# Performance work log

Hardware: AMD Instinct MI355X
Metric: run time of the kernel (lower is better)

Reference implementation:

```python
import jax, jax.numpy as jnp
import numpy as np

N_ITER = 2


def _ssn_iter(pixel_features, sh, sw, n_iter=N_ITER):
    """Faithful JAX port of ssn_iter: returns dense abs_affinity (B, ns, N).

    dist[b,k,p] = ||pix[b,:,p] - spix[b,:,cand_k(p)]||^2 over the 3x3 superpixel
    neighborhood of each pixel's initial label; invalid candidates get +inf
    (softmax -> 0), matching the CUDA PairwiseDistFunction + mask semantics.
    """
    B, C, H, W = pixel_features.shape
    nsh, nsw = H // sh, W // sw
    ns = nsh * nsw
    N = H * W

    # calc_init_centroid: adaptive_avg_pool2d == block mean when divisible
    spix = pixel_features.reshape(B, C, nsh, sh, nsw, sw).mean(axis=(3, 5)).reshape(B, C, ns)

    # init_label_map via nearest interpolation == (row//sh)*nsw + col//sw
    r0 = jnp.repeat(jnp.arange(H) // sh, W)            # (N,) superpixel row of each pixel
    c0 = jnp.tile(jnp.arange(W) // sw, H)              # (N,) superpixel col

    # 9 candidate offsets, ordered as [r-nsw, r, r+nsw] with r in [-1,0,1]
    dr = jnp.repeat(jnp.arange(-1, 2), 3)              # (9,)
    dc = jnp.tile(jnp.arange(-1, 2), 3)                # (9,)
    rr = r0[None, :] + dr[:, None]                     # (9, N)
    cc = c0[None, :] + dc[:, None]                     # (9, N)
    valid = (rr >= 0) & (rr < nsh) & (cc >= 0) & (cc < nsw)   # (9, N)
    sidx = jnp.clip(rr * nsw + cc, 0, ns - 1)          # (9, N) candidate superpixel ids
    pidx = jnp.broadcast_to(jnp.arange(N), (9, N))     # (9, N) pixel ids

    pf = pixel_features.reshape(B, C, N)

    def scatter_dense(a):  # a: (9, N) affinity -> dense (ns, N)
        return jnp.zeros((ns, N), a.dtype).at[sidx, pidx].add(a)

    abs_aff = None
    for k in range(n_iter):
        g = spix[:, :, sidx.reshape(-1)].reshape(B, C, 9, N)          # gather candidates
        d = ((pf[:, :, None, :] - g) ** 2).sum(axis=1)                # (B, 9, N)
        d = jnp.where(valid[None], d, jnp.inf)
        aff = jax.nn.softmax(-d, axis=1)                              # invalid -> 0
        aff = jnp.where(valid[None], aff, 0.0)
        abs_aff = jax.vmap(scatter_dense)(aff)                        # (B, ns, N)
        if k < n_iter - 1:
            num = jnp.einsum('bsn,bcn->bsc', abs_aff, pf)             # dense bmm
            den = abs_aff.sum(axis=2)[..., None] + 1e-16
            spix = (num / den).transpose(0, 2, 1)                     # (B, C, ns)
    return abs_aff


def setup_inputs() -> dict:
    key = jax.random.key(0)
    x = jax.random.normal(key, (2, 64, 320, 320), dtype=jnp.float32)
    return {"pixel_features": x, "stoken_h": 16, "stoken_w": 16}


def reference(pixel_features, stoken_h, stoken_w):
    return _ssn_iter(pixel_features, stoken_h, stoken_w, N_ITER)
```

## Files before the change

kernel.cpp:

```cpp
#include <hip/hip_runtime.h>

#define KB   2
#define KC   64
#define KH   320
#define KW   320
#define KSH  16
#define KSW  16
#define KNSH 20
#define KNSW 20
#define KNS  400
#define KN   102400

#define TOTF4  20480000u
#define Z1     6800000u
#define Z2     13640000u
#define NZA    1024
#define NZB    1248
#define NZC    1248
#define NCOMPA 2560
#define NCOMP  800

typedef float float4v __attribute__((ext_vector_type(4)));

__global__ __launch_bounds__(320) void block_mean_kernel(
    const float* __restrict__ pf, float* __restrict__ spix,
    float* __restrict__ outz) {
  if (blockIdx.x < NZA) {
    unsigned tid = blockIdx.x * 320u + threadIdx.x;
    const unsigned stride = NZA * 320u;
    float4v z = (float4v)(0.f);
    float4v* o = (float4v*)outz;
    for (unsigned i = tid; i < Z1; i += stride)
      __builtin_nontemporal_store(z, &o[i]);
    return;
  }
  int wg = blockIdx.x - NZA;
  int rb = wg % KNSH;
  int c  = (wg / KNSH) % KC;
  int b  = wg / (KNSH * KC);
  int t  = threadIdx.x;

  const float* row0 = pf + ((size_t)(b * KC + c) * KH + rb * KSH) * KW;
  float acc = 0.f;
#pragma unroll
  for (int i = 0; i < KSH; ++i) acc += row0[i * KW + t];

#pragma unroll
  for (int off = 8; off > 0; off >>= 1) acc += __shfl_down(acc, off, 16);

  if ((t & 15) == 0)
    spix[(b * KC + c) * KNS + rb * KNSW + (t >> 4)] = acc * (1.0f / (KSH * KSW));
}

__global__ __launch_bounds__(256) void dist_partial_kernel(
    const float* __restrict__ pf, const float* __restrict__ spix,
    float* __restrict__ part, float* __restrict__ den,
    float* __restrict__ outz) {
  if (blockIdx.x < NZB) {
    unsigned tid = blockIdx.x * 256u + threadIdx.x;
    const unsigned stride = NZB * 256u;
    float4v z = (float4v)(0.f);
    float4v* o = (float4v*)outz;
    for (unsigned i = Z1 + tid; i < Z2; i += stride)
      __builtin_nontemporal_store(z, &o[i]);
    return;
  }

  __shared__ float scand[9][KC];
  __shared__ __align__(16) float aff_s[9][256];
  __shared__ float part_s[9][64];
  __shared__ float den_s[9];

  int wg = blockIdx.x - NZB;
  int s  = wg % KNS;
  int b  = wg / KNS;
  int sr = s / KNSW, sc = s % KNSW;
  int t  = threadIdx.x;

  for (int idx = t; idx < 9 * KC; idx += 256) {
    int k = idx >> 6, c = idx & 63;
    int rr = sr + k / 3 - 1, cc = sc + k % 3 - 1;
    float v = 0.f;
    if (rr >= 0 && rr < KNSH && cc >= 0 && cc < KNSW)
      v = spix[(b * KC + c) * KNS + rr * KNSW + cc];
    scand[k][c] = v;
  }
  __syncthreads();

  int ti = t >> 4, tj = t & 15;
  int p = (sr * KSH + ti) * KW + sc * KSW + tj;
  const float* pfp = pf + (size_t)b * KC * KN + p;

  float d[9];
#pragma unroll
  for (int k = 0; k < 9; ++k) d[k] = 0.f;
  for (int c = 0; c < KC; ++c) {
    float x = pfp[(size_t)c * KN];
#pragma unroll
    for (int k = 0; k < 9; ++k) {
      float df = x - scand[k][c];
      d[k] = fmaf(df, df, d[k]);
    }
  }
  float m = 3.4e38f;
#pragma unroll
  for (int k = 0; k < 9; ++k) {
    int rr = sr + k / 3 - 1, cc = sc + k % 3 - 1;
    if (rr >= 0 && rr < KNSH && cc >= 0 && cc < KNSW) m = fminf(m, d[k]);
  }
  float e[9];
  float sum = 0.f;
#pragma unroll
  for (int k = 0; k < 9; ++k) {
    int rr = sr + k / 3 - 1, cc = sc + k % 3 - 1;
    bool valid = (rr >= 0 && rr < KNSH && cc >= 0 && cc < KNSW);
    e[k] = valid ? __expf(m - d[k]) : 0.f;
    sum += e[k];
  }
  float inv = 1.0f / sum;
#pragma unroll
  for (int k = 0; k < 9; ++k) aff_s[k][t] = e[k] * inv;
  __syncthreads();

  int w = t >> 6, l = t & 63;
  int li = l >> 2, lj4 = (l & 3) * 4;
  const float* pfb = pf + ((size_t)b * KC + w * 16) * KN
                   + (sr * KSH + li) * KW + sc * KSW + lj4;

  const float4v a0 = *(const float4v*)(&aff_s[0][l * 4]);
  const float4v a1 = *(const float4v*)(&aff_s[1][l * 4]);
  const float4v a2 = *(const float4v*)(&aff_s[2][l * 4]);
  const float4v a3 = *(const float4v*)(&aff_s[3][l * 4]);
  const float4v a4 = *(const float4v*)(&aff_s[4][l * 4]);
  const float4v a5 = *(const float4v*)(&aff_s[5][l * 4]);
  const float4v a6 = *(const float4v*)(&aff_s[6][l * 4]);
  const float4v a7 = *(const float4v*)(&aff_s[7][l * 4]);
  const float4v a8 = *(const float4v*)(&aff_s[8][l * 4]);

  if (w == 0) {
#define DENK(k, av)                                                       \
    {                                                                     \
      float dv = (av.x + av.y) + (av.z + av.w);                           \
      _Pragma("unroll")                                                   \
      for (int off = 32; off > 0; off >>= 1) dv += __shfl_xor(dv, off, 64); \
      if (l == 0) den_s[k] = dv;                                          \
    }
    DENK(0, a0) DENK(1, a1) DENK(2, a2) DENK(3, a3) DENK(4, a4)
    DENK(5, a5) DENK(6, a6) DENK(7, a7) DENK(8, a8)
#undef DENK
  }

#pragma unroll
  for (int cb = 0; cb < 4; ++cb) {
    float4v x0 = *(const float4v*)(pfb + (size_t)(cb * 4 + 0) * KN);
    float4v x1 = *(const float4v*)(pfb + (size_t)(cb * 4 + 1) * KN);
    float4v x2 = *(const float4v*)(pfb + (size_t)(cb * 4 + 2) * KN);
    float4v x3 = *(const float4v*)(pfb + (size_t)(cb * 4 + 3) * KN);

    float acc[4][9];
#define DOTS(c, xv)                                                        \
    acc[c][0] = fmaf(xv.x, a0.x, fmaf(xv.y, a0.y, fmaf(xv.z, a0.z, xv.w * a0.w))); \
    acc[c][1] = fmaf(xv.x, a1.x, fmaf(xv.y, a1.y, fmaf(xv.z, a1.z, xv.w * a1.w))); \
    acc[c][2] = fmaf(xv.x, a2.x, fmaf(xv.y, a2.y, fmaf(xv.z, a2.z, xv.w * a2.w))); \
    acc[c][3] = fmaf(xv.x, a3.x, fmaf(xv.y, a3.y, fmaf(xv.z, a3.z, xv.w * a3.w))); \
    acc[c][4] = fmaf(xv.x, a4.x, fmaf(xv.y, a4.y, fmaf(xv.z, a4.z, xv.w * a4.w))); \
    acc[c][5] = fmaf(xv.x, a5.x, fmaf(xv.y, a5.y, fmaf(xv.z, a5.z, xv.w * a5.w))); \
    acc[c][6] = fmaf(xv.x, a6.x, fmaf(xv.y, a6.y, fmaf(xv.z, a6.z, xv.w * a6.w))); \
    acc[c][7] = fmaf(xv.x, a7.x, fmaf(xv.y, a7.y, fmaf(xv.z, a7.z, xv.w * a7.w))); \
    acc[c][8] = fmaf(xv.x, a8.x, fmaf(xv.y, a8.y, fmaf(xv.z, a8.z, xv.w * a8.w)));
    DOTS(0, x0) DOTS(1, x1) DOTS(2, x2) DOTS(3, x3)
#undef DOTS

#pragma unroll
    for (int off = 32; off > 0; off >>= 1)
#pragma unroll
      for (int c = 0; c < 4; ++c)
#pragma unroll
        for (int k = 0; k < 9; ++k)
          acc[c][k] += __shfl_xor(acc[c][k], off, 64);

    if (l == 0) {
#pragma unroll
      for (int c = 0; c < 4; ++c)
#pragma unroll
        for (int k = 0; k < 9; ++k)
          part_s[k][w * 16 + cb * 4 + c] = acc[c][k];
    }
  }
  __syncthreads();

  size_t base = ((size_t)b * KNS + s) * 9;
  for (int idx = t; idx < 9 * 64; idx += 256)
    part[base * 64 + idx] = part_s[idx >> 6][idx & 63];
  if (t < 9) den[base + t] = den_s[t];
}

__global__ __launch_bounds__(256) void dist_band_kernel(
    const float* __restrict__ pf, const float* __restrict__ part,
    const float* __restrict__ den, float* __restrict__ out) {
  if (blockIdx.x < NZC) {
    unsigned tid = blockIdx.x * 256u + threadIdx.x;
    const unsigned stride = NZC * 256u;
    float4v z = (float4v)(0.f);
    float4v* o = (float4v*)out;
    for (unsigned i = Z2 + tid; i < TOTF4; i += stride) {
      unsigned orow = i / 25600u;
      unsigned f4   = i - orow * 25600u;
      unsigned s    = orow % KNS;
      unsigned p    = f4 * 4u;
      int sr = (int)(s / KNSW), sc = (int)(s % KNSW);
      int r0 = (int)(p / 5120u);
      int c0 = (int)((p % KW) >> 4);
      int dr = sr - r0, dc = sc - c0;
      if (dr < -1 || dr > 1 || dc < -1 || dc > 1)
        __builtin_nontemporal_store(z, &o[i]);
    }
    return;
  }

  __shared__ float scand[9][KC];

  int wg = blockIdx.x - NZC;
  int s  = wg % KNS;
  int b  = wg / KNS;
  int sr = s / KNSW, sc = s % KNSW;
  int t  = threadIdx.x;

  for (int idx = t; idx < 9 * KC; idx += 256) {
    int k = idx >> 6, c = idx & 63;
    int nr = sr + k / 3 - 1, nc = sc + k % 3 - 1;
    float v = 0.f;
    if (nr >= 0 && nr < KNSH && nc >= 0 && nc < KNSW) {
      float num = 0.f, dsum = 0.f;
#pragma unroll
      for (int j = 0; j < 9; ++j) {
        int rr = nr + j / 3 - 1, cc = nc + j % 3 - 1;
        if (rr >= 0 && rr < KNSH && cc >= 0 && cc < KNSW) {
          size_t base = ((size_t)b * KNS + rr * KNSW + cc) * 9 + (8 - j);
          num  += part[base * 64 + c];
          dsum += den[base];
        }
      }
      v = num / (dsum + 1e-16f);
    }
    scand[k][c] = v;
  }
  __syncthreads();

  int i = t >> 4, j = t & 15;
  int p = (sr * KSH + i) * KW + sc * KSW + j;
  const float* pfb = pf + (size_t)b * KC * KN + p;

  float d[9];
#pragma unroll
  for (int k = 0; k < 9; ++k) d[k] = 0.f;

  for (int c = 0; c < KC; ++c) {
    float x = pfb[(size_t)c * KN];
#pragma unroll
    for (int k = 0; k < 9; ++k) {
      float df = x - scand[k][c];
      d[k] = fmaf(df, df, d[k]);
    }
  }

  float m = 3.4e38f;
#pragma unroll
  for (int k = 0; k < 9; ++k) {
    int rr = sr + k / 3 - 1, cc = sc + k % 3 - 1;
    bool valid = (rr >= 0 && rr < KNSH && cc >= 0 && cc < KNSW);
    if (valid) m = fminf(m, d[k]);
  }
  float e[9];
  float sum = 0.f;
#pragma unroll
  for (int k = 0; k < 9; ++k) {
    int rr = sr + k / 3 - 1, cc = sc + k % 3 - 1;
    bool valid = (rr >= 0 && rr < KNSH && cc >= 0 && cc < KNSW);
    e[k] = valid ? __expf(m - d[k]) : 0.f;
    sum += e[k];
  }
  float inv = 1.0f / sum;

#pragma unroll
  for (int k = 0; k < 9; ++k) {
    int rr = sr + k / 3 - 1, cc = sc + k % 3 - 1;
    if (rr >= 0 && rr < KNSH && cc >= 0 && cc < KNSW)
      __builtin_nontemporal_store(e[k] * inv,
          out + ((size_t)b * KNS + rr * KNSW + cc) * KN + p);
  }
}

extern "C" void kernel_launch(void* const* d_in, const int* in_sizes, int n_in,
                              void* d_out, int out_size, void* d_ws, size_t ws_size,
                              hipStream_t stream) {
  const float* pf = (const float*)d_in[0];
  float* out = (float*)d_out;

  float* spix0 = (float*)d_ws;
  float* partw = spix0 + (size_t)KB * KC * KNS;
  float* denw  = partw + (size_t)KB * KNS * 9 * 64;

  block_mean_kernel<<<NZA + NCOMPA, 320, 0, stream>>>(pf, spix0, out);
  dist_partial_kernel<<<NZB + NCOMP, 256, 0, stream>>>(pf, spix0, partw, denw, out);
  dist_band_kernel<<<NZC + NCOMP, 256, 0, stream>>>(pf, partw, denw, out);
}
```

Measured before the change: 144.9 us.

## Move output zeroing out of band kernel and dispatch compute blocks first

The pass that zero-fills the huge dense output is now split evenly between the first two kernels, each covering half the buffer unconditionally. The third kernel no longer zeroes anything and only writes the banded affinities. Compute workgroups now sit at the low block indices so they are dispatched ahead of the zero-fill blocks. This drops the per-element band test and its integer divisions from the zero loop, but the band region is now written twice and the last kernel's compute no longer overlaps with any zeroing.

```diff
diff --git a/kernel.cpp b/kernel.cpp
--- a/kernel.cpp
+++ b/kernel.cpp
@@ -12,29 +12,27 @@
 #define KN   102400
 
 #define TOTF4  20480000u
-#define Z1     6800000u
-#define Z2     13640000u
+#define HALF4  10240000u
+#define NCOMPA 2560
 #define NZA    1024
+#define NCOMP  800
 #define NZB    1248
-#define NZC    1248
-#define NCOMPA 2560
-#define NCOMP  800
 
 typedef float float4v __attribute__((ext_vector_type(4)));
 
 __global__ __launch_bounds__(320) void block_mean_kernel(
     const float* __restrict__ pf, float* __restrict__ spix,
     float* __restrict__ outz) {
-  if (blockIdx.x < NZA) {
-    unsigned tid = blockIdx.x * 320u + threadIdx.x;
+  if (blockIdx.x >= NCOMPA) {
+    unsigned tid = (blockIdx.x - NCOMPA) * 320u + threadIdx.x;
     const unsigned stride = NZA * 320u;
     float4v z = (float4v)(0.f);
     float4v* o = (float4v*)outz;
-    for (unsigned i = tid; i < Z1; i += stride)
+    for (unsigned i = tid; i < HALF4; i += stride)
       __builtin_nontemporal_store(z, &o[i]);
     return;
   }
-  int wg = blockIdx.x - NZA;
+  int wg = blockIdx.x;
   int rb = wg % KNSH;
   int c  = (wg / KNSH) % KC;
   int b  = wg / (KNSH * KC);
@@ -56,12 +54,12 @@
     const float* __restrict__ pf, const float* __restrict__ spix,
     float* __restrict__ part, float* __restrict__ den,
     float* __restrict__ outz) {
-  if (blockIdx.x < NZB) {
-    unsigned tid = blockIdx.x * 256u + threadIdx.x;
+  if (blockIdx.x >= NCOMP) {
+    unsigned tid = (blockIdx.x - NCOMP) * 256u + threadIdx.x;
     const unsigned stride = NZB * 256u;
     float4v z = (float4v)(0.f);
     float4v* o = (float4v*)outz;
-    for (unsigned i = Z1 + tid; i < Z2; i += stride)
+    for (unsigned i = HALF4 + tid; i < TOTF4; i += stride)
       __builtin_nontemporal_store(z, &o[i]);
     return;
   }
@@ -71,7 +69,7 @@
   __shared__ float part_s[9][64];
   __shared__ float den_s[9];
 
-  int wg = blockIdx.x - NZB;
+  int wg = blockIdx.x;
   int s  = wg % KNS;
   int b  = wg / KNS;
   int sr = s / KNSW, sc = s % KNSW;
@@ -198,29 +196,9 @@
 __global__ __launch_bounds__(256) void dist_band_kernel(
     const float* __restrict__ pf, const float* __restrict__ part,
     const float* __restrict__ den, float* __restrict__ out) {
-  if (blockIdx.x < NZC) {
-    unsigned tid = blockIdx.x * 256u + threadIdx.x;
-    const unsigned stride = NZC * 256u;
-    float4v z = (float4v)(0.f);
-    float4v* o = (float4v*)out;
-    for (unsigned i = Z2 + tid; i < TOTF4; i += stride) {
-      unsigned orow = i / 25600u;
-      unsigned f4   = i - orow * 25600u;
-      unsigned s    = orow % KNS;
-      unsigned p    = f4 * 4u;
-      int sr = (int)(s / KNSW), sc = (int)(s % KNSW);
-      int r0 = (int)(p / 5120u);
-      int c0 = (int)((p % KW) >> 4);
-      int dr = sr - r0, dc = sc - c0;
-      if (dr < -1 || dr > 1 || dc < -1 || dc > 1)
-        __builtin_nontemporal_store(z, &o[i]);
-    }
-    return;
-  }
-
   __shared__ float scand[9][KC];
 
-  int wg = blockIdx.x - NZC;
+  int wg = blockIdx.x;
   int s  = wg % KNS;
   int b  = wg / KNS;
   int sr = s / KNSW, sc = s % KNSW;
@@ -301,7 +279,7 @@
   float* partw = spix0 + (size_t)KB * KC * KNS;
   float* denw  = partw + (size_t)KB * KNS * 9 * 64;
 
-  block_mean_kernel<<<NZA + NCOMPA, 320, 0, stream>>>(pf, spix0, out);
-  dist_partial_kernel<<<NZB + NCOMP, 256, 0, stream>>>(pf, spix0, partw, denw, out);
-  dist_band_kernel<<<NZC + NCOMP, 256, 0, stream>>>(pf, partw, denw, out);
-}
+  block_mean_kernel<<<NCOMPA + NZA, 320, 0, stream>>>(pf, spix0, out);
+  dist_partial_kernel<<<NCOMP + NZB, 256, 0, stream>>>(pf, spix0, partw, denw, out);
+  dist_band_kernel<<<NCOMP, 256, 0, stream>>>(pf, partw, denw, out);
+}
```

New measurement: 137.3 us. 1.06x faster.
